# Kernel tuning notes

Hardware: AMD Instinct MI355X
Metric: run time of the kernel (lower is better)

## Reference

```python
import jax, jax.numpy as jnp
import numpy as np

N, E = 50000, 600000
DIN, D, C = 239, 128, 2
NEG_SLOPE_MLP = 0.01   # nn.LeakyReLU default
NEG_SLOPE_ATT = 0.2    # GATConv default


def leaky(x, s):
    return jnp.where(x >= 0, x, s * x)


def setup_inputs() -> dict:
    key = jax.random.key(0)
    ks = jax.random.split(key, 12)
    sc = lambda d: 1.0 / np.sqrt(d)
    return {
        "x": jax.random.normal(ks[0], (N, DIN), jnp.float32),
        "edge_index": jax.random.randint(ks[1], (2, E), 0, N, jnp.int32),
        "edge_type": jax.random.randint(ks[2], (E,), 0, 4, jnp.int32),
        "W_in": jax.random.normal(ks[3], (DIN, D), jnp.float32) * sc(DIN),
        "b_in": jnp.zeros((D,), jnp.float32),
        "W_gat": jax.random.normal(ks[4], (D, D), jnp.float32) * sc(D),
        "att_src": jax.random.normal(ks[5], (D,), jnp.float32) * sc(D),
        "att_dst": jax.random.normal(ks[6], (D,), jnp.float32) * sc(D),
        "b_gat": jnp.zeros((D,), jnp.float32),
        "W_h": jax.random.normal(ks[7], (D, D), jnp.float32) * sc(D),
        "b_h": jnp.zeros((D,), jnp.float32),
        "W_out": jax.random.normal(ks[8], (D, C), jnp.float32) * sc(D),
        "b_out": jnp.zeros((C,), jnp.float32),
    }


def reference(x, edge_index, edge_type, W_in, b_in, W_gat, att_src, att_dst,
              b_gat, W_h, b_h, W_out, b_out):
    # input encoder: Linear + LeakyReLU
    h = leaky(x @ W_in + b_in, NEG_SLOPE_MLP)                      # [N, D]

    # GATConv (heads=1): add self loops, edge attention, segment softmax over dst
    loops = jnp.arange(N, dtype=edge_index.dtype)
    src = jnp.concatenate([edge_index[0], loops])                  # [E+N]
    dst = jnp.concatenate([edge_index[1], loops])

    g = h @ W_gat                                                  # [N, D]
    a_src = g @ att_src                                            # [N]
    a_dst = g @ att_dst                                            # [N]
    e = leaky(a_src[src] + a_dst[dst], NEG_SLOPE_ATT)              # [E+N]

    m = jax.ops.segment_max(e, dst, num_segments=N)                # self-loops => no empty segs
    w = jnp.exp(e - m[dst])
    z = jax.ops.segment_sum(w, dst, num_segments=N)
    alpha = w / z[dst]                                             # [E+N]

    out = jax.ops.segment_sum(alpha[:, None] * g[src], dst, num_segments=N) + b_gat

    # dropout is identity in eval mode
    h2 = leaky(out @ W_h + b_h, NEG_SLOPE_MLP)
    return h2 @ W_out + b_out                                      # [N, C]
```

## Files before the change

kernel.cpp:

```cpp
#include <hip/hip_runtime.h>

#define NNODE 50000
#define NEDGE 600000
#define KDIN  239
#define DDIM  128
#define NTILES 3125
#define NBG   782
#define NBUCK 256
#define BSZ   196
#define NPB   128
#define CHP   4688

typedef _Float16 half8 __attribute__((ext_vector_type(8)));
typedef _Float16 half4 __attribute__((ext_vector_type(4)));
typedef __attribute__((ext_vector_type(4))) float f32x4;

__device__ __forceinline__ ushort f2h(float f){
  union { _Float16 h; ushort u; } c; c.h = (_Float16)f; return c.u;
}

__global__ __launch_bounds__(256) void pre_k(
    const float* __restrict__ W_in, const float* __restrict__ W_gat, const float* __restrict__ W_h,
    ushort* __restrict__ BfA, ushort* __restrict__ BfB, ushort* __restrict__ BfC,
    const int* __restrict__ ei, int* __restrict__ cpart)
{
  __shared__ int hb[NBUCK];
  const int b = blockIdx.x, t = threadIdx.x;
  if (b < NPB){
    hb[t] = 0;
    __syncthreads();
    const int e0 = b*CHP, e1 = min(NEDGE, e0+CHP);
    for (int e=e0+t; e<e1; e+=256){
      int dst = min(max(ei[NEDGE+e],0), NNODE-1);
      atomicAdd(&hb[dst/BSZ], 1);
    }
    __syncthreads();
    cpart[b*NBUCK + t] = hb[t];
  } else if (b < NPB + 128){
    int idx = (b-NPB)*256 + t; int n = idx >> 8, k = idx & 255;
    BfA[idx] = (k < KDIN) ? f2h(W_in[(size_t)k*DDIM + n]) : (ushort)0;
  } else if (b < NPB + 192){
    int idx = (b-NPB-128)*256 + t; int n = idx >> 7, k = idx & 127;
    BfB[idx] = f2h(W_gat[(size_t)k*DDIM + n]);
  } else {
    int idx = (b-NPB-192)*256 + t; int n = idx >> 7, k = idx & 127;
    BfC[idx] = f2h(W_h[(size_t)k*DDIM + n]);
  }
}

__global__ __launch_bounds__(256, 3) void gemmAB_k(
    const float* __restrict__ x, const ushort* __restrict__ BfA,
    const ushort* __restrict__ BfB, const float* __restrict__ b_in,
    ushort* __restrict__ gf,
    const float* __restrict__ vs, const float* __restrict__ vd,
    float* __restrict__ os, float* __restrict__ od,
    float* __restrict__ bms, float* __restrict__ bmd,
    const int* __restrict__ ei, const int* __restrict__ cpart, int* __restrict__ pairs,
    int* __restrict__ gmS)
{
  __shared__ __attribute__((aligned(16))) ushort Bs[128*128];
  __shared__ __attribute__((aligned(16))) ushort ht[4][16*128];
  if (blockIdx.x < NPB){
    int* cur = (int*)Bs;
    int* scn = ((int*)Bs) + NBUCK;
    const int pb = blockIdx.x, t = threadIdx.x;
    int tot = 0, before = 0;
    #pragma unroll 8
    for (int i=0;i<NPB;i++){
      const int c = cpart[i*NBUCK + t];
      if (i < pb) before += c;
      tot += c;
    }
    scn[t] = tot;
    __syncthreads();
    #pragma unroll
    for (int off=1; off<NBUCK; off<<=1){
      int v = (t>=off) ? scn[t-off] : 0;
      __syncthreads();
      scn[t] += v;
      __syncthreads();
    }
    const int S = scn[t] - tot;
    cur[t] = S + before;
    if (pb == 0) gmS[t] = S;
    __syncthreads();
    const int e0 = pb*CHP, e1 = min(NEDGE, e0+CHP);
    for (int e=e0+t; e<e1; e+=256){
      int dst = min(max(ei[NEDGE+e],0), NNODE-1);
      int src = min(max(ei[e],0), NNODE-1);
      int bk = (unsigned)dst / BSZ;
      int pos = atomicAdd(&cur[bk], 1);
      pairs[pos] = src | ((dst - bk*BSZ) << 16);
    }
    return;
  }
  const int lane = threadIdx.x & 63;
  const int wave = threadIdx.x >> 6;
  const int q = lane >> 4, c = lane & 15;
  const int tile = (blockIdx.x - NPB)*4 + wave;
  const bool act = tile < NTILES;
  const int rowBase = tile*16;
  const int swz = (c&7)<<4;
  f32x4 acc[8];
  half8 af[8];
  if (act){
    const float* __restrict__ ap = x + (size_t)(rowBase + c)*KDIN;
    #pragma unroll
    for (int s=0;s<7;s++){
      const float* __restrict__ p = ap + s*32 + q*8;
      #pragma unroll
      for (int i=0;i<8;i++) af[s][i] = (_Float16)p[i];
    }
    #pragma unroll
    for (int i=0;i<8;i++){
      const int k = 224 + q*8 + i;
      af[7][i] = (_Float16)((k < KDIN) ? ap[k] : 0.f);
    }
    #pragma unroll
    for (int t=0;t<8;t++) acc[t] = (f32x4){0.f,0.f,0.f,0.f};
  }
  #pragma unroll
  for (int H=0; H<2; ++H){
    #pragma unroll
    for (int it=0; it<8; ++it){
      const int idx = it*256 + threadIdx.x;
      const int row = idx >> 4, sl = (idx & 15)*16;
      const half8 v = *(const half8*)(BfA + (size_t)row*256 + H*128 + (idx & 15)*8);
      *(half8*)((char*)Bs + row*256 + (sl ^ ((row&7)<<4))) = v;
    }
    __syncthreads();
    if (act){
      const char* __restrict__ bsl = (const char*)Bs + c*256;
      #pragma unroll
      for (int s=0;s<4;s++){
        const int so = (s*64 + q*16) ^ swz;
        #pragma unroll
        for (int t=0;t<8;t++){
          const half8 bf = *(const half8*)(bsl + t*16*256 + so);
          acc[t] = __builtin_amdgcn_mfma_f32_16x16x32_f16(af[H*4+s], bf, acc[t], 0,0,0);
        }
      }
    }
    __syncthreads();
  }
  if (act){
    char* __restrict__ hw = (char*)&ht[wave][0];
    #pragma unroll
    for (int t=0;t<8;t++){
      const int col = 16*t + c;
      const float bv = b_in[col];
      #pragma unroll
      for (int r=0;r<4;r++){
        const int row = q*4 + r;
        float v = acc[t][r] + bv;
        v = (v >= 0.f) ? v : 0.01f*v;
        *(_Float16*)(hw + ((row*256 + col*2) ^ ((row&7)<<4))) = (_Float16)v;
      }
    }
  }
  #pragma unroll
  for (int it=0; it<8; ++it){
    const int idx = it*256 + threadIdx.x;
    const int row = idx >> 4, sl = (idx & 15)*16;
    const half8 v = *(const half8*)(BfB + (size_t)idx*8);
    *(half8*)((char*)Bs + row*256 + (sl ^ ((row&7)<<4))) = v;
  }
  __syncthreads();
  if (!act) return;
  half8 af2[4];
  const char* __restrict__ hr = (const char*)&ht[wave][0] + c*256;
  #pragma unroll
  for (int s=0;s<4;s++) af2[s] = *(const half8*)(hr + ((s*64 + q*16) ^ swz));
  #pragma unroll
  for (int t=0;t<8;t++) acc[t] = (f32x4){0.f,0.f,0.f,0.f};
  const char* __restrict__ bsl2 = (const char*)Bs + c*256;
  #pragma unroll
  for (int s=0;s<4;s++){
    const int so = (s*64 + q*16) ^ swz;
    #pragma unroll
    for (int t=0;t<8;t++){
      const half8 bf = *(const half8*)(bsl2 + t*16*256 + so);
      acc[t] = __builtin_amdgcn_mfma_f32_16x16x32_f16(af2[s], bf, acc[t], 0,0,0);
    }
  }
  float pr0[4] = {0,0,0,0}, pr1[4] = {0,0,0,0};
  #pragma unroll
  for (int t=0;t<8;t++){
    const int col = 16*t + c;
    const float va = vs[col], vb = vd[col];
    #pragma unroll
    for (int r=0;r<4;r++){
      const int row = rowBase + q*4 + r;
      const float v = acc[t][r];
      gf[(size_t)row*DDIM + col] = f2h(v);
      pr0[r] += v*va; pr1[r] += v*vb;
    }
  }
  float lmax_s = -3.0e38f, lmax_d = -3.0e38f;
  #pragma unroll
  for (int r=0;r<4;r++){
    float s0 = pr0[r], s1 = pr1[r];
    s0 += __shfl_xor(s0,8); s1 += __shfl_xor(s1,8);
    s0 += __shfl_xor(s0,4); s1 += __shfl_xor(s1,4);
    s0 += __shfl_xor(s0,2); s1 += __shfl_xor(s1,2);
    s0 += __shfl_xor(s0,1); s1 += __shfl_xor(s1,1);
    lmax_s = fmaxf(lmax_s, s0); lmax_d = fmaxf(lmax_d, s1);
    if (c == 0){
      const int row = rowBase + q*4 + r;
      os[row] = s0; od[row] = s1;
    }
  }
  #pragma unroll
  for (int off=32; off>0; off>>=1){
    lmax_s = fmaxf(lmax_s, __shfl_xor(lmax_s, off));
    lmax_d = fmaxf(lmax_d, __shfl_xor(lmax_d, off));
  }
  if (lane == 0){ bms[tile] = lmax_s; bmd[tile] = lmax_d; }
}

__global__ __launch_bounds__(256) void fine_k(const int* __restrict__ pairs,
    const int* __restrict__ gmS, int* __restrict__ offs, int* __restrict__ degv,
    int* __restrict__ es, const float* __restrict__ bms, const float* __restrict__ bmd,
    float* __restrict__ gmf)
{
  __shared__ int fh[256];
  __shared__ int sc[256];
  const int b = blockIdx.x, t = threadIdx.x;
  if (b == NBUCK){
    float ms = -3.0e38f, md = -3.0e38f;
    for (int i=t; i<NTILES; i+=256){ ms = fmaxf(ms, bms[i]); md = fmaxf(md, bmd[i]); }
    #pragma unroll
    for (int off=32; off>0; off>>=1){
      ms = fmaxf(ms, __shfl_xor(ms, off));
      md = fmaxf(md, __shfl_xor(md, off));
    }
    float* red = (float*)fh;
    const int w = t >> 6;
    if ((t & 63) == 0){ red[w] = ms; red[4+w] = md; }
    __syncthreads();
    if (t == 0){
      gmf[0] = fmaxf(fmaxf(red[0],red[1]), fmaxf(red[2],red[3]));
      gmf[1] = fmaxf(fmaxf(red[4],red[5]), fmaxf(red[6],red[7]));
    }
    return;
  }
  const int s0 = gmS[b];
  const int s1 = (b < NBUCK-1) ? gmS[b+1] : NEDGE;
  fh[t] = 0;
  __syncthreads();
  for (int i=s0+t; i<s1; i+=256)
    atomicAdd(&fh[pairs[i] >> 16], 1);
  __syncthreads();
  const int deg = fh[t];
  sc[t] = deg;
  __syncthreads();
  #pragma unroll
  for (int off=1; off<256; off<<=1){
    int v = (t>=off) ? sc[t-off] : 0;
    __syncthreads();
    sc[t] += v;
    __syncthreads();
  }
  const int excl = sc[t] - deg;
  const int dst = b*BSZ + t;
  if (t < BSZ && dst < NNODE){ offs[dst] = s0 + excl; degv[dst] = deg; }
  fh[t] = s0 + excl;
  __syncthreads();
  for (int i=s0+t; i<s1; i+=256){
    const int p = pairs[i];
    const int pos = atomicAdd(&fh[p >> 16], 1);
    es[pos] = p & 0xFFFF;
  }
}

__global__ __launch_bounds__(256) void agg_k(const ushort* __restrict__ gf,
    const int* __restrict__ offs, const int* __restrict__ degv,
    const int* __restrict__ es,
    const float* __restrict__ a_src, const float* __restrict__ a_dst,
    const float* __restrict__ gmf, const float* __restrict__ b_gat,
    ushort* __restrict__ og)
{
  const int lane = threadIdx.x & 63;
  const int half = lane >> 5, li = lane & 31;
  const int dst = blockIdx.x*8 + (threadIdx.x >> 6)*2 + half;
  if (dst >= NNODE) return;
  float M = gmf[0] + gmf[1];
  M = (M >= 0.f) ? M : 0.2f*M;
  const int start = offs[dst];
  const int deg = degv[dst];
  const int* __restrict__ bin = es + start;
  const float ad = a_dst[dst];
  f32x4 a0={0,0,0,0}, a1={0,0,0,0}, a2={0,0,0,0}, a3={0,0,0,0};
  float w0s=0.f, w1s=0.f, w2s=0.f, w3s=0.f;
  int j = 0;
  for (; j+3 < deg; j += 4){
    const int i0=bin[j], i1=bin[j+1], i2=bin[j+2], i3=bin[j+3];
    float e0=a_src[i0]+ad; e0=(e0>=0.f)?e0:0.2f*e0;
    float e1=a_src[i1]+ad; e1=(e1>=0.f)?e1:0.2f*e1;
    float e2=a_src[i2]+ad; e2=(e2>=0.f)?e2:0.2f*e2;
    float e3=a_src[i3]+ad; e3=(e3>=0.f)?e3:0.2f*e3;
    const float w0=__expf(e0-M), w1=__expf(e1-M), w2=__expf(e2-M), w3=__expf(e3-M);
    const half4 g0 = *(const half4*)(gf + (size_t)i0*DDIM + li*4);
    const half4 g1 = *(const half4*)(gf + (size_t)i1*DDIM + li*4);
    const half4 g2 = *(const half4*)(gf + (size_t)i2*DDIM + li*4);
    const half4 g3 = *(const half4*)(gf + (size_t)i3*DDIM + li*4);
    #pragma unroll
    for (int i=0;i<4;i++){
      a0[i] += w0*(float)g0[i]; a1[i] += w1*(float)g1[i];
      a2[i] += w2*(float)g2[i]; a3[i] += w3*(float)g3[i];
    }
    w0s += w0; w1s += w1; w2s += w2; w3s += w3;
  }
  for (; j < deg; ++j){
    const int si = bin[j];
    float e0=a_src[si]+ad; e0=(e0>=0.f)?e0:0.2f*e0;
    const float w = __expf(e0-M);
    const half4 gv = *(const half4*)(gf + (size_t)si*DDIM + li*4);
    #pragma unroll
    for (int i=0;i<4;i++) a0[i] += w*(float)gv[i];
    w0s += w;
  }
  {
    float evs=a_src[dst]+ad; evs=(evs>=0.f)?evs:0.2f*evs;
    const float w = __expf(evs-M);
    const half4 gv = *(const half4*)(gf + (size_t)dst*DDIM + li*4);
    #pragma unroll
    for (int i=0;i<4;i++) a0[i] += w*(float)gv[i];
    w0s += w;
  }
  const float inv = 1.f/(w0s+w1s+w2s+w3s);
  const float4 bg = *(const float4*)&b_gat[li*4];
  ushort4 o;
  o.x = f2h((a0[0]+a1[0]+a2[0]+a3[0])*inv + bg.x);
  o.y = f2h((a0[1]+a1[1]+a2[1]+a3[1])*inv + bg.y);
  o.z = f2h((a0[2]+a1[2]+a2[2]+a3[2])*inv + bg.z);
  o.w = f2h((a0[3]+a1[3]+a2[3]+a3[3])*inv + bg.w);
  *(ushort4*)(og + (size_t)dst*DDIM + li*4) = o;
}

__global__ __launch_bounds__(256, 4) void gemmC_k(
    const ushort* __restrict__ Af, const ushort* __restrict__ Btf,
    const float* __restrict__ bias, float* __restrict__ outf,
    const float* __restrict__ Wo, const float* __restrict__ bo)
{
  constexpr int Kpad = 128, Kb = 256;
  __shared__ __attribute__((aligned(16))) ushort Bs[128*Kpad];
  #pragma unroll
  for (int it=0; it<8; ++it){
    const int idx = it*256 + threadIdx.x;
    const int row = idx >> 4, sl = (idx & 15)*16;
    const half8 v = *(const half8*)(Btf + (size_t)idx*8);
    *(half8*)((char*)Bs + row*Kb + (sl ^ ((row&7)<<4))) = v;
  }
  __syncthreads();
  const int lane = threadIdx.x & 63;
  const int wave = threadIdx.x >> 6;
  const int q = lane >> 4, c = lane & 15;
  const int tile = blockIdx.x*4 + wave;
  if (tile >= NTILES) return;
  const int rowBase = tile*16;
  half8 af[4];
  const ushort* __restrict__ ap = Af + (size_t)(rowBase + c)*Kpad + q*8;
  #pragma unroll
  for (int s=0;s<4;s++) af[s] = *(const half8*)(ap + s*32);
  f32x4 acc[8];
  #pragma unroll
  for (int t=0;t<8;t++) acc[t] = (f32x4){0.f,0.f,0.f,0.f};
  const int swz = (c&7)<<4;
  const char* __restrict__ bsl = (const char*)Bs + c*Kb;
  #pragma unroll
  for (int s=0;s<4;s++){
    const int so = (s*64 + q*16) ^ swz;
    #pragma unroll
    for (int t=0;t<8;t++){
      const half8 bf = *(const half8*)(bsl + t*16*Kb + so);
      acc[t] = __builtin_amdgcn_mfma_f32_16x16x32_f16(af[s], bf, acc[t], 0,0,0);
    }
  }
  float pr0[4] = {0,0,0,0}, pr1[4] = {0,0,0,0};
  #pragma unroll
  for (int t=0;t<8;t++){
    const int col = 16*t + c;
    const float bv = bias[col];
    const float va = Wo[2*col], vb = Wo[2*col+1];
    #pragma unroll
    for (int r=0;r<4;r++){
      float v = acc[t][r] + bv;
      v = (v >= 0.f) ? v : 0.01f*v;
      pr0[r] += v*va; pr1[r] += v*vb;
    }
  }
  #pragma unroll
  for (int r=0;r<4;r++){
    float s0 = pr0[r], s1 = pr1[r];
    s0 += __shfl_xor(s0,8); s1 += __shfl_xor(s1,8);
    s0 += __shfl_xor(s0,4); s1 += __shfl_xor(s1,4);
    s0 += __shfl_xor(s0,2); s1 += __shfl_xor(s1,2);
    s0 += __shfl_xor(s0,1); s1 += __shfl_xor(s1,1);
    if (c == 0){
      const int row = rowBase + q*4 + r;
      float2 y2; y2.x = s0 + bo[0]; y2.y = s1 + bo[1];
      *(float2*)&outf[(size_t)row*2] = y2;
    }
  }
}

extern "C" void kernel_launch(void* const* d_in, const int* in_sizes, int n_in,
                              void* d_out, int out_size, void* d_ws, size_t ws_size,
                              hipStream_t stream)
{
  const float* x       = (const float*)d_in[0];
  const int*   ei      = (const int*)d_in[1];
  const float* W_in    = (const float*)d_in[3];
  const float* b_in    = (const float*)d_in[4];
  const float* W_gat   = (const float*)d_in[5];
  const float* att_src = (const float*)d_in[6];
  const float* att_dst = (const float*)d_in[7];
  const float* b_gat   = (const float*)d_in[8];
  const float* W_h     = (const float*)d_in[9];
  const float* b_h     = (const float*)d_in[10];
  const float* W_out   = (const float*)d_in[11];
  const float* b_out   = (const float*)d_in[12];

  char* ws = (char*)d_ws;
  ushort*   gf     = (ushort*)  (ws + 0);
  ushort*   og     = (ushort*)  (ws + 12800000);
  ushort*   BfA    = (ushort*)  (ws + 25600000);
  ushort*   BfB    = (ushort*)  (ws + 25800000);
  ushort*   BfC    = (ushort*)  (ws + 25900000);
  int*      cpart  = (int*)     (ws + 26000000);
  int*      pairs  = (int*)     (ws + 26300000);
  int*      es     = (int*)     (ws + 28700000);
  int*      offs   = (int*)     (ws + 31100000);
  int*      degv   = (int*)     (ws + 31300000);
  float*    a_src  = (float*)   (ws + 31500000);
  float*    a_dst  = (float*)   (ws + 31700000);
  float*    gm     = (float*)   (ws + 31900000);
  int*      gmS    = (int*)     (ws + 31900128);
  float*    bmaxS  = (float*)   (ws + 32000000);
  float*    bmaxD  = (float*)   (ws + 32016000);

  pre_k<<<NPB + 256, 256, 0, stream>>>(W_in, W_gat, W_h, BfA, BfB, BfC, ei, cpart);
  gemmAB_k<<<NPB + NBG, 256, 0, stream>>>(x, BfA, BfB, b_in, gf,
      att_src, att_dst, a_src, a_dst, bmaxS, bmaxD, ei, cpart, pairs, gmS);
  fine_k<<<NBUCK + 1, 256, 0, stream>>>(pairs, gmS, offs, degv, es, bmaxS, bmaxD, gm);
  agg_k<<<6250, 256, 0, stream>>>(gf, offs, degv, es, a_src, a_dst, gm, b_gat, og);
  gemmC_k<<<NBG, 256, 0, stream>>>(og, BfC, b_h, (float*)d_out, W_out, b_out);
}
```

Measured before the change: 173.4 us.

## Fuse CSR fine-sort and GAT aggregation into one bucket kernel with LDS edge lists

Merges the per-bucket counting-sort kernel and the aggregation kernel into a single 1024-thread kernel per destination bucket. Edge source lists are kept in LDS when the bucket fits, and the global max reduction is recomputed in every block, so the offs/degv/es round-trips and one launch are removed. The cost is parallelism: aggregation now runs on only 256 blocks of 32 half-wave slots instead of 6250 blocks, which may leave the GPU underoccupied for a latency-bound gather.

New measurement: 171.0 us. About the same (-1.4%).

```diff
diff --git a/kernel.cpp b/kernel.cpp
--- a/kernel.cpp
+++ b/kernel.cpp
@@ -10,6 +10,7 @@
 #define BSZ   196
 #define NPB   128
 #define CHP   4688
+#define ESCAP 4096
 
 typedef _Float16 half8 __attribute__((ext_vector_type(8)));
 typedef _Float16 half4 __attribute__((ext_vector_type(4)));
@@ -218,124 +219,128 @@
   if (lane == 0){ bms[tile] = lmax_s; bmd[tile] = lmax_d; }
 }
 
-__global__ __launch_bounds__(256) void fine_k(const int* __restrict__ pairs,
-    const int* __restrict__ gmS, int* __restrict__ offs, int* __restrict__ degv,
-    int* __restrict__ es, const float* __restrict__ bms, const float* __restrict__ bmd,
-    float* __restrict__ gmf)
+__global__ __launch_bounds__(1024, 2) void fineagg_k(
+    const int* __restrict__ pairs, const int* __restrict__ gmS,
+    int* __restrict__ es, const ushort* __restrict__ gf,
+    const float* __restrict__ a_src, const float* __restrict__ a_dst,
+    const float* __restrict__ bms, const float* __restrict__ bmd,
+    const float* __restrict__ b_gat, ushort* __restrict__ og)
 {
   __shared__ int fh[256];
-  __shared__ int sc[256];
+  __shared__ int sc2[256];
+  __shared__ int offL[256];
+  __shared__ int degL[256];
+  __shared__ int esL[ESCAP];
+  __shared__ float Msh;
   const int b = blockIdx.x, t = threadIdx.x;
-  if (b == NBUCK){
-    float ms = -3.0e38f, md = -3.0e38f;
-    for (int i=t; i<NTILES; i+=256){ ms = fmaxf(ms, bms[i]); md = fmaxf(md, bmd[i]); }
-    #pragma unroll
-    for (int off=32; off>0; off>>=1){
-      ms = fmaxf(ms, __shfl_xor(ms, off));
-      md = fmaxf(md, __shfl_xor(md, off));
-    }
-    float* red = (float*)fh;
-    const int w = t >> 6;
-    if ((t & 63) == 0){ red[w] = ms; red[4+w] = md; }
-    __syncthreads();
-    if (t == 0){
-      gmf[0] = fmaxf(fmaxf(red[0],red[1]), fmaxf(red[2],red[3]));
-      gmf[1] = fmaxf(fmaxf(red[4],red[5]), fmaxf(red[6],red[7]));
-    }
-    return;
-  }
+  float ms = -3.0e38f, md = -3.0e38f;
+  for (int i=t; i<NTILES; i+=1024){ ms = fmaxf(ms, bms[i]); md = fmaxf(md, bmd[i]); }
+  #pragma unroll
+  for (int off=32; off>0; off>>=1){
+    ms = fmaxf(ms, __shfl_xor(ms, off));
+    md = fmaxf(md, __shfl_xor(md, off));
+  }
+  float* red = (float*)sc2;
+  const int w = t >> 6;
+  if ((t & 63) == 0){ red[w] = ms; red[16+w] = md; }
+  __syncthreads();
+  if (t == 0){
+    float As = red[0], Ad = red[16];
+    #pragma unroll
+    for (int i=1;i<16;i++){ As = fmaxf(As, red[i]); Ad = fmaxf(Ad, red[16+i]); }
+    float M = As + Ad;
+    Msh = (M >= 0.f) ? M : 0.2f*M;
+  }
+  if (t < 256) fh[t] = 0;
+  __syncthreads();
   const int s0 = gmS[b];
   const int s1 = (b < NBUCK-1) ? gmS[b+1] : NEDGE;
-  fh[t] = 0;
-  __syncthreads();
-  for (int i=s0+t; i<s1; i+=256)
+  const bool fit = (s1 - s0) <= ESCAP;
+  for (int i=s0+t; i<s1; i+=1024)
     atomicAdd(&fh[pairs[i] >> 16], 1);
   __syncthreads();
-  const int deg = fh[t];
-  sc[t] = deg;
+  int deg = 0;
+  if (t < 256){ deg = fh[t]; sc2[t] = deg; }
   __syncthreads();
   #pragma unroll
   for (int off=1; off<256; off<<=1){
-    int v = (t>=off) ? sc[t-off] : 0;
-    __syncthreads();
-    sc[t] += v;
-    __syncthreads();
-  }
-  const int excl = sc[t] - deg;
-  const int dst = b*BSZ + t;
-  if (t < BSZ && dst < NNODE){ offs[dst] = s0 + excl; degv[dst] = deg; }
-  fh[t] = s0 + excl;
-  __syncthreads();
-  for (int i=s0+t; i<s1; i+=256){
+    int v = (t < 256 && t >= off) ? sc2[t-off] : 0;
+    __syncthreads();
+    if (t < 256) sc2[t] += v;
+    __syncthreads();
+  }
+  if (t < 256){
+    const int excl = sc2[t] - deg;
+    offL[t] = excl;
+    degL[t] = deg;
+    fh[t] = excl;
+  }
+  __syncthreads();
+  for (int i=s0+t; i<s1; i+=1024){
     const int p = pairs[i];
     const int pos = atomicAdd(&fh[p >> 16], 1);
-    es[pos] = p & 0xFFFF;
-  }
-}
-
-__global__ __launch_bounds__(256) void agg_k(const ushort* __restrict__ gf,
-    const int* __restrict__ offs, const int* __restrict__ degv,
-    const int* __restrict__ es,
-    const float* __restrict__ a_src, const float* __restrict__ a_dst,
-    const float* __restrict__ gmf, const float* __restrict__ b_gat,
-    ushort* __restrict__ og)
-{
-  const int lane = threadIdx.x & 63;
+    if (fit) esL[pos] = p & 0xFFFF;
+    else     es[s0 + pos] = p & 0xFFFF;
+  }
+  __syncthreads();
+  const float M = Msh;
+  const int lane = t & 63;
   const int half = lane >> 5, li = lane & 31;
-  const int dst = blockIdx.x*8 + (threadIdx.x >> 6)*2 + half;
-  if (dst >= NNODE) return;
-  float M = gmf[0] + gmf[1];
-  M = (M >= 0.f) ? M : 0.2f*M;
-  const int start = offs[dst];
-  const int deg = degv[dst];
-  const int* __restrict__ bin = es + start;
-  const float ad = a_dst[dst];
-  f32x4 a0={0,0,0,0}, a1={0,0,0,0}, a2={0,0,0,0}, a3={0,0,0,0};
-  float w0s=0.f, w1s=0.f, w2s=0.f, w3s=0.f;
-  int j = 0;
-  for (; j+3 < deg; j += 4){
-    const int i0=bin[j], i1=bin[j+1], i2=bin[j+2], i3=bin[j+3];
-    float e0=a_src[i0]+ad; e0=(e0>=0.f)?e0:0.2f*e0;
-    float e1=a_src[i1]+ad; e1=(e1>=0.f)?e1:0.2f*e1;
-    float e2=a_src[i2]+ad; e2=(e2>=0.f)?e2:0.2f*e2;
-    float e3=a_src[i3]+ad; e3=(e3>=0.f)?e3:0.2f*e3;
-    const float w0=__expf(e0-M), w1=__expf(e1-M), w2=__expf(e2-M), w3=__expf(e3-M);
-    const half4 g0 = *(const half4*)(gf + (size_t)i0*DDIM + li*4);
-    const half4 g1 = *(const half4*)(gf + (size_t)i1*DDIM + li*4);
-    const half4 g2 = *(const half4*)(gf + (size_t)i2*DDIM + li*4);
-    const half4 g3 = *(const half4*)(gf + (size_t)i3*DDIM + li*4);
-    #pragma unroll
-    for (int i=0;i<4;i++){
-      a0[i] += w0*(float)g0[i]; a1[i] += w1*(float)g1[i];
-      a2[i] += w2*(float)g2[i]; a3[i] += w3*(float)g3[i];
-    }
-    w0s += w0; w1s += w1; w2s += w2; w3s += w3;
-  }
-  for (; j < deg; ++j){
-    const int si = bin[j];
-    float e0=a_src[si]+ad; e0=(e0>=0.f)?e0:0.2f*e0;
-    const float w = __expf(e0-M);
-    const half4 gv = *(const half4*)(gf + (size_t)si*DDIM + li*4);
-    #pragma unroll
-    for (int i=0;i<4;i++) a0[i] += w*(float)gv[i];
-    w0s += w;
-  }
-  {
-    float evs=a_src[dst]+ad; evs=(evs>=0.f)?evs:0.2f*evs;
-    const float w = __expf(evs-M);
-    const half4 gv = *(const half4*)(gf + (size_t)dst*DDIM + li*4);
-    #pragma unroll
-    for (int i=0;i<4;i++) a0[i] += w*(float)gv[i];
-    w0s += w;
-  }
-  const float inv = 1.f/(w0s+w1s+w2s+w3s);
+  const int slot = (t >> 6)*2 + half;
   const float4 bg = *(const float4*)&b_gat[li*4];
-  ushort4 o;
-  o.x = f2h((a0[0]+a1[0]+a2[0]+a3[0])*inv + bg.x);
-  o.y = f2h((a0[1]+a1[1]+a2[1]+a3[1])*inv + bg.y);
-  o.z = f2h((a0[2]+a1[2]+a2[2]+a3[2])*inv + bg.z);
-  o.w = f2h((a0[3]+a1[3]+a2[3]+a3[3])*inv + bg.w);
-  *(ushort4*)(og + (size_t)dst*DDIM + li*4) = o;
+  for (int d = slot; d < BSZ; d += 32){
+    const int dst = b*BSZ + d;
+    if (dst >= NNODE) continue;
+    const int start = offL[d];
+    const int dg = degL[d];
+    const int* __restrict__ bin = fit ? (esL + start) : (es + s0 + start);
+    const float ad = a_dst[dst];
+    f32x4 a0={0,0,0,0}, a1={0,0,0,0}, a2={0,0,0,0}, a3={0,0,0,0};
+    float w0s=0.f, w1s=0.f, w2s=0.f, w3s=0.f;
+    int j = 0;
+    for (; j+3 < dg; j += 4){
+      const int i0=bin[j], i1=bin[j+1], i2=bin[j+2], i3=bin[j+3];
+      float e0=a_src[i0]+ad; e0=(e0>=0.f)?e0:0.2f*e0;
+      float e1=a_src[i1]+ad; e1=(e1>=0.f)?e1:0.2f*e1;
+      float e2=a_src[i2]+ad; e2=(e2>=0.f)?e2:0.2f*e2;
+      float e3=a_src[i3]+ad; e3=(e3>=0.f)?e3:0.2f*e3;
+      const float w0=__expf(e0-M), w1=__expf(e1-M), w2=__expf(e2-M), w3=__expf(e3-M);
+      const half4 g0 = *(const half4*)(gf + (size_t)i0*DDIM + li*4);
+      const half4 g1 = *(const half4*)(gf + (size_t)i1*DDIM + li*4);
+      const half4 g2 = *(const half4*)(gf + (size_t)i2*DDIM + li*4);
+      const half4 g3 = *(const half4*)(gf + (size_t)i3*DDIM + li*4);
+      #pragma unroll
+      for (int i=0;i<4;i++){
+        a0[i] += w0*(float)g0[i]; a1[i] += w1*(float)g1[i];
+        a2[i] += w2*(float)g2[i]; a3[i] += w3*(float)g3[i];
+      }
+      w0s += w0; w1s += w1; w2s += w2; w3s += w3;
+    }
+    for (; j < dg; ++j){
+      const int si = bin[j];
+      float e0=a_src[si]+ad; e0=(e0>=0.f)?e0:0.2f*e0;
+      const float w = __expf(e0-M);
+      const half4 gv = *(const half4*)(gf + (size_t)si*DDIM + li*4);
+      #pragma unroll
+      for (int i=0;i<4;i++) a0[i] += w*(float)gv[i];
+      w0s += w;
+    }
+    {
+      float evs=a_src[dst]+ad; evs=(evs>=0.f)?evs:0.2f*evs;
+      const float w = __expf(evs-M);
+      const half4 gv = *(const half4*)(gf + (size_t)dst*DDIM + li*4);
+      #pragma unroll
+      for (int i=0;i<4;i++) a0[i] += w*(float)gv[i];
+      w0s += w;
+    }
+    const float inv = 1.f/(w0s+w1s+w2s+w3s);
+    ushort4 o;
+    o.x = f2h((a0[0]+a1[0]+a2[0]+a3[0])*inv + bg.x);
+    o.y = f2h((a0[1]+a1[1]+a2[1]+a3[1])*inv + bg.y);
+    o.z = f2h((a0[2]+a1[2]+a2[2]+a3[2])*inv + bg.z);
+    o.w = f2h((a0[3]+a1[3]+a2[3]+a3[3])*inv + bg.w);
+    *(ushort4*)(og + (size_t)dst*DDIM + li*4) = o;
+  }
 }
 
 __global__ __launch_bounds__(256, 4) void gemmC_k(
@@ -431,19 +436,16 @@
   int*      cpart  = (int*)     (ws + 26000000);
   int*      pairs  = (int*)     (ws + 26300000);
   int*      es     = (int*)     (ws + 28700000);
-  int*      offs   = (int*)     (ws + 31100000);
-  int*      degv   = (int*)     (ws + 31300000);
-  float*    a_src  = (float*)   (ws + 31500000);
-  float*    a_dst  = (float*)   (ws + 31700000);
-  float*    gm     = (float*)   (ws + 31900000);
-  int*      gmS    = (int*)     (ws + 31900128);
-  float*    bmaxS  = (float*)   (ws + 32000000);
-  float*    bmaxD  = (float*)   (ws + 32016000);
+  float*    a_src  = (float*)   (ws + 31100000);
+  float*    a_dst  = (float*)   (ws + 31300000);
+  int*      gmS    = (int*)     (ws + 31500000);
+  float*    bmaxS  = (float*)   (ws + 31600000);
+  float*    bmaxD  = (float*)   (ws + 31616000);
 
   pre_k<<<NPB + 256, 256, 0, stream>>>(W_in, W_gat, W_h, BfA, BfB, BfC, ei, cpart);
   gemmAB_k<<<NPB + NBG, 256, 0, stream>>>(x, BfA, BfB, b_in, gf,
       att_src, att_dst, a_src, a_dst, bmaxS, bmaxD, ei, cpart, pairs, gmS);
-  fine_k<<<NBUCK + 1, 256, 0, stream>>>(pairs, gmS, offs, degv, es, bmaxS, bmaxD, gm);
-  agg_k<<<6250, 256, 0, stream>>>(gf, offs, degv, es, a_src, a_dst, gm, b_gat, og);
+  fineagg_k<<<NBUCK, 1024, 0, stream>>>(pairs, gmS, es, gf, a_src, a_dst,
+      bmaxS, bmaxD, b_gat, og);
   gemmC_k<<<NBG, 256, 0, stream>>>(og, BfC, b_h, (float*)d_out, W_out, b_out);
 }
```
